# Kernel optimization log

Hardware: AMD Instinct MI355X
Metric: run time of the kernel (lower is better)

## Reference

```python
import jax, jax.numpy as jnp
import numpy as np

STRIDE = 1
PADDING = (1, 1, 1, 1)  # (left, right, top, bottom), as in torch F.pad for last two dims
NEG_INF = -jnp.inf


def maxplus_conv2d(x, kernel, stride=STRIDE):
    """Tropical (max-plus) conv2d, groups=1.
    x: [B, C, H, W] (already padded), kernel: [O, C, kh, kw].
    out[b,o,h,w] = max_{c,ki,kj} x[b,c,h*s+ki,w*s+kj] + kernel[o,c,ki,kj]
    """
    B, C, H, W = x.shape
    O, Cg, kh, kw = kernel.shape
    Ho = (H - kh) // stride + 1
    Wo = (W - kw) // stride + 1
    out = jnp.full((B, O, Ho, Wo), NEG_INF, dtype=x.dtype)
    # Loop over the small, fixed kernel taps (kh*kw = 9); reductions over the
    # channel axis stay fully vectorized and fuse into a single add+reduce-max.
    for ki in range(kh):
        for kj in range(kw):
            xs = x[:, :, ki:ki + Ho * stride:stride, kj:kj + Wo * stride:stride]  # [B,C,Ho,Wo]
            cand = jnp.max(xs[:, None, :, :, :] + kernel[None, :, :, ki, kj][:, :, :, None, None], axis=2)
            out = jnp.maximum(out, cand)
    return out


def setup_inputs() -> dict:
    key = jax.random.key(0)
    kx, kk = jax.random.split(key)
    x = jax.random.normal(kx, (8, 64, 64, 64), dtype=jnp.float32)
    kernel = jax.random.normal(kk, (64, 64, 3, 3), dtype=jnp.float32) * 0.1
    return {"x": x, "kernel": kernel}


def reference(x, kernel):
    left, right, top, bottom = PADDING
    # MaxPlus semifield: pad with the additive identity of max, i.e. -inf
    xp = jnp.pad(x, ((0, 0), (0, 0), (top, bottom), (left, right)), mode="constant", constant_values=NEG_INF)
    return maxplus_conv2d(xp, kernel, STRIDE)
```

## Files before the change

kernel.cpp:

```cpp
#include <hip/hip_runtime.h>

#define NEG_INF (-__builtin_huge_valf())

#define CCH   4
#define HB    4
#define ROWS  (HB + 2)
#define XSTR  64
#define ESTR  40
#define SLOTS 6

__global__ __launch_bounds__(64, 4)
void maxplus_conv2d_kernel(const float* __restrict__ x,
                           const float* __restrict__ kern,
                           float* __restrict__ out) {
    __shared__ float xs[CCH * ROWS * XSTR];
    __shared__ float es[CCH * ROWS * ESTR];

    const int tid = threadIdx.x;
    const int wg  = tid & 15;
    const int hr  = tid >> 4;
    const int w0  = wg << 2;

    const int h_base = blockIdx.x * HB;
    const int b      = blockIdx.y;
    const int o_base = blockIdx.z << 1;

    const float* xb = x + (size_t)b * 64 * 64 * 64;
    const float* gsrc[SLOTS];
    float*       xdst[SLOTS];
    float*       edst[SLOTS];
    bool         vmask[SLOTS];
#pragma unroll
    for (int k = 0; k < SLOTS; ++k) {
        int rowid = k * 4 + hr;
        int cl    = rowid / ROWS;
        int r     = rowid - cl * ROWS;
        int gh    = h_base + r - 1;
        bool valid = (unsigned)gh < 64u;
        int  ghc   = valid ? gh : 0;
        gsrc[k]  = xb + ((size_t)cl * 64 + ghc) * 64 + wg * 4;
        xdst[k]  = &xs[rowid * XSTR + wg * 4];
        edst[k]  = &es[rowid * ESTR + wg];
        vmask[k] = valid;
    }

    if (tid < CCH * ROWS) {
        es[tid * ESTR + 0]  = NEG_INF;
        es[tid * ESTR + 34] = NEG_INF;
    }

    float acc[2][4];
#pragma unroll
    for (int oo = 0; oo < 2; ++oo)
#pragma unroll
        for (int wi = 0; wi < 4; ++wi)
            acc[oo][wi] = NEG_INF;

    float4 R[SLOTS];
#pragma unroll
    for (int k = 0; k < SLOTS; ++k) R[k] = *(const float4*)gsrc[k];

#pragma unroll 1
    for (int cc = 0; cc < 64; cc += CCH) {
        __syncthreads();

#pragma unroll
        for (int k = 0; k < SLOTS; ++k) {
            float4 v = R[k];
            if (!vmask[k]) v = make_float4(NEG_INF, NEG_INF, NEG_INF, NEG_INF);
            *(float4*)xdst[k] = v;
            edst[k][1]  = v.w;
            edst[k][18] = v.x;
        }

        __syncthreads();

        if (cc + CCH < 64) {
#pragma unroll
            for (int k = 0; k < SLOTS; ++k) {
                gsrc[k] += CCH * 64 * 64;
                R[k] = *(const float4*)gsrc[k];
            }
        }

        float kv[CCH][2][9];
#pragma unroll
        for (int cl = 0; cl < CCH; ++cl)
#pragma unroll
            for (int oo = 0; oo < 2; ++oo) {
                const float* kp = kern + ((size_t)(o_base + oo) * 64 + (cc + cl)) * 9;
#pragma unroll
                for (int t = 0; t < 9; ++t) kv[cl][oo][t] = kp[t];
            }

#pragma unroll
        for (int cl = 0; cl < CCH; ++cl) {
            float xv[3][6];
#pragma unroll
            for (int r = 0; r < 3; ++r) {
                const int rowid = cl * ROWS + hr + r;
                float4 m = *(const float4*)(&xs[rowid * XSTR + w0]);
                const float* ep = &es[rowid * ESTR + wg];
                xv[r][0] = ep[0];
                xv[r][5] = ep[19];
                xv[r][1] = m.x; xv[r][2] = m.y; xv[r][3] = m.z; xv[r][4] = m.w;
            }

#pragma unroll
            for (int oo = 0; oo < 2; ++oo) {
                const float* k9 = kv[cl][oo];
#pragma unroll
                for (int wi = 0; wi < 4; ++wi) {
                    float m = acc[oo][wi];
                    float t0 = xv[0][wi + 0] + k9[0];
                    float t1 = xv[0][wi + 1] + k9[1];
                    m = fmaxf(m, fmaxf(t0, t1));
                    t0 = xv[0][wi + 2] + k9[2];
                    t1 = xv[1][wi + 0] + k9[3];
                    m = fmaxf(m, fmaxf(t0, t1));
                    t0 = xv[1][wi + 1] + k9[4];
                    t1 = xv[1][wi + 2] + k9[5];
                    m = fmaxf(m, fmaxf(t0, t1));
                    t0 = xv[2][wi + 0] + k9[6];
                    t1 = xv[2][wi + 1] + k9[7];
                    m = fmaxf(m, fmaxf(t0, t1));
                    m = fmaxf(m, xv[2][wi + 2] + k9[8]);
                    acc[oo][wi] = m;
                }
            }
        }
    }

    const int h = h_base + hr;
#pragma unroll
    for (int oo = 0; oo < 2; ++oo) {
        float4 v = make_float4(acc[oo][0], acc[oo][1], acc[oo][2], acc[oo][3]);
        *(float4*)(out + ((((size_t)b * 64 + (o_base + oo)) * 64 + h) * 64 + w0)) = v;
    }
}

extern "C" void kernel_launch(void* const* d_in, const int* in_sizes, int n_in,
                              void* d_out, int out_size, void* d_ws, size_t ws_size,
                              hipStream_t stream) {
    const float* x    = (const float*)d_in[0];
    const float* kern = (const float*)d_in[1];
    float* out = (float*)d_out;

    dim3 grid(16, 8, 32);
    dim3 block(64);
    maxplus_conv2d_kernel<<<grid, block, 0, stream>>>(x, kern, out);
}
```

Baseline: 110.2 us.

## Share input tile across four waves and fetch halo columns via DPP

Each block now holds four waves, and each wave computes two output channels from a single shared input tile, so input traffic per output channel drops by a factor of four. The channel chunk per stage is doubled to 8. The separate shared-memory edge array is removed and left/right neighbour columns are read across lanes with DPP row shifts that fill -inf at the row boundaries. Padding rows are now written once as -inf for edge blocks instead of being masked on every store. The cost is a larger block, twice the shared memory per block, a split inner loop to limit registers, and fewer blocks in the grid.

After: 123.0 us. 1.12x slower.

```diff
diff --git a/kernel.cpp b/kernel.cpp
--- a/kernel.cpp
+++ b/kernel.cpp
@@ -1,52 +1,60 @@
 #include <hip/hip_runtime.h>
 
 #define NEG_INF (-__builtin_huge_valf())
+#define NEG_INF_BITS 0xFF800000
 
-#define CCH   4
-#define HB    4
-#define ROWS  (HB + 2)
-#define XSTR  64
-#define ESTR  40
-#define SLOTS 6
+#define CCH    8
+#define HB     4
+#define ROWS   (HB + 2)
+#define NROW   (CCH * ROWS)
+#define XSTR   64
+#define SLOTS  3
+#define OW     4
 
-__global__ __launch_bounds__(64, 4)
+template <int CTRL>
+__device__ __forceinline__ float dpp_neighbor(float v) {
+    return __int_as_float(__builtin_amdgcn_update_dpp(
+        (int)NEG_INF_BITS, __float_as_int(v), CTRL, 0xF, 0xF, false));
+}
+
+__global__ __launch_bounds__(256, 4)
 void maxplus_conv2d_kernel(const float* __restrict__ x,
                            const float* __restrict__ kern,
                            float* __restrict__ out) {
-    __shared__ float xs[CCH * ROWS * XSTR];
-    __shared__ float es[CCH * ROWS * ESTR];
+    __shared__ float xs[NROW * XSTR];
 
-    const int tid = threadIdx.x;
-    const int wg  = tid & 15;
-    const int hr  = tid >> 4;
-    const int w0  = wg << 2;
+    const int tid  = threadIdx.x;
+    const int lane = tid & 63;
+    const int wave = __builtin_amdgcn_readfirstlane(tid >> 6);
+    const int wg   = lane & 15;
+    const int hr   = lane >> 4;
+    const int w0   = wg << 2;
 
     const int h_base = blockIdx.x * HB;
     const int b      = blockIdx.y;
-    const int o_base = blockIdx.z << 1;
+    const int o0     = blockIdx.z * (OW * 2) + wave * 2;
 
-    const float* xb = x + (size_t)b * 64 * 64 * 64;
+    if (h_base == 0 || h_base == 60) {
+        for (int k = tid; k < NROW * XSTR; k += 256)
+            xs[k] = NEG_INF;
+    }
+
+    const float* xb = x + (size_t)b * (64 * 64 * 64);
     const float* gsrc[SLOTS];
     float*       xdst[SLOTS];
-    float*       edst[SLOTS];
-    bool         vmask[SLOTS];
+    bool         sval[SLOTS];
 #pragma unroll
-    for (int k = 0; k < SLOTS; ++k) {
-        int rowid = k * 4 + hr;
+    for (int s = 0; s < SLOTS; ++s) {
+        int idx   = s * 256 + tid;
+        int rowid = idx >> 4;
+        int wgp   = idx & 15;
         int cl    = rowid / ROWS;
         int r     = rowid - cl * ROWS;
         int gh    = h_base + r - 1;
-        bool valid = (unsigned)gh < 64u;
-        int  ghc   = valid ? gh : 0;
-        gsrc[k]  = xb + ((size_t)cl * 64 + ghc) * 64 + wg * 4;
-        xdst[k]  = &xs[rowid * XSTR + wg * 4];
-        edst[k]  = &es[rowid * ESTR + wg];
-        vmask[k] = valid;
-    }
-
-    if (tid < CCH * ROWS) {
-        es[tid * ESTR + 0]  = NEG_INF;
-        es[tid * ESTR + 34] = NEG_INF;
+        bool v    = (unsigned)gh < 64u;
+        gsrc[s] = xb + ((size_t)cl * 64 + (v ? gh : 0)) * 64 + wgp * 4;
+        xdst[s] = &xs[rowid * XSTR + wgp * 4];
+        sval[s] = v;
     }
 
     float acc[2][4];
@@ -58,74 +66,71 @@
 
     float4 R[SLOTS];
 #pragma unroll
-    for (int k = 0; k < SLOTS; ++k) R[k] = *(const float4*)gsrc[k];
+    for (int s = 0; s < SLOTS; ++s) R[s] = *(const float4*)gsrc[s];
+
+    const float* kpw = kern + (size_t)o0 * (64 * 9);
 
 #pragma unroll 1
     for (int cc = 0; cc < 64; cc += CCH) {
         __syncthreads();
-
 #pragma unroll
-        for (int k = 0; k < SLOTS; ++k) {
-            float4 v = R[k];
-            if (!vmask[k]) v = make_float4(NEG_INF, NEG_INF, NEG_INF, NEG_INF);
-            *(float4*)xdst[k] = v;
-            edst[k][1]  = v.w;
-            edst[k][18] = v.x;
-        }
-
+        for (int s = 0; s < SLOTS; ++s)
+            if (sval[s]) *(float4*)xdst[s] = R[s];
         __syncthreads();
 
         if (cc + CCH < 64) {
 #pragma unroll
-            for (int k = 0; k < SLOTS; ++k) {
-                gsrc[k] += CCH * 64 * 64;
-                R[k] = *(const float4*)gsrc[k];
+            for (int s = 0; s < SLOTS; ++s) {
+                gsrc[s] += CCH * 64 * 64;
+                R[s] = *(const float4*)gsrc[s];
             }
         }
 
-        float kv[CCH][2][9];
+#pragma unroll 1
+        for (int half = 0; half < 2; ++half) {
+            float kv[4][2][9];
 #pragma unroll
-        for (int cl = 0; cl < CCH; ++cl)
+            for (int cl = 0; cl < 4; ++cl)
 #pragma unroll
-            for (int oo = 0; oo < 2; ++oo) {
-                const float* kp = kern + ((size_t)(o_base + oo) * 64 + (cc + cl)) * 9;
+                for (int oo = 0; oo < 2; ++oo) {
+                    const float* kp = kpw + ((size_t)oo * 64 + (cc + half * 4 + cl)) * 9;
 #pragma unroll
-                for (int t = 0; t < 9; ++t) kv[cl][oo][t] = kp[t];
-            }
+                    for (int t = 0; t < 9; ++t) kv[cl][oo][t] = kp[t];
+                }
 
 #pragma unroll
-        for (int cl = 0; cl < CCH; ++cl) {
-            float xv[3][6];
+            for (int cl = 0; cl < 4; ++cl) {
+                const int rbase = (half * 4 + cl) * ROWS + hr;
+                float xv[3][6];
 #pragma unroll
-            for (int r = 0; r < 3; ++r) {
-                const int rowid = cl * ROWS + hr + r;
-                float4 m = *(const float4*)(&xs[rowid * XSTR + w0]);
-                const float* ep = &es[rowid * ESTR + wg];
-                xv[r][0] = ep[0];
-                xv[r][5] = ep[19];
-                xv[r][1] = m.x; xv[r][2] = m.y; xv[r][3] = m.z; xv[r][4] = m.w;
-            }
+                for (int r = 0; r < 3; ++r) {
+                    float4 m = *(const float4*)(&xs[(rbase + r) * XSTR + w0]);
+                    xv[r][0] = dpp_neighbor<0x111>(m.w);
+                    xv[r][1] = m.x; xv[r][2] = m.y; xv[r][3] = m.z; xv[r][4] = m.w;
+                    xv[r][5] = dpp_neighbor<0x101>(m.x);
+                }
 
 #pragma unroll
-            for (int oo = 0; oo < 2; ++oo) {
-                const float* k9 = kv[cl][oo];
+                for (int oo = 0; oo < 2; ++oo) {
+                    const float* k9 = kv[cl][oo];
 #pragma unroll
-                for (int wi = 0; wi < 4; ++wi) {
-                    float m = acc[oo][wi];
-                    float t0 = xv[0][wi + 0] + k9[0];
-                    float t1 = xv[0][wi + 1] + k9[1];
-                    m = fmaxf(m, fmaxf(t0, t1));
-                    t0 = xv[0][wi + 2] + k9[2];
-                    t1 = xv[1][wi + 0] + k9[3];
-                    m = fmaxf(m, fmaxf(t0, t1));
-                    t0 = xv[1][wi + 1] + k9[4];
-                    t1 = xv[1][wi + 2] + k9[5];
-                    m = fmaxf(m, fmaxf(t0, t1));
-                    t0 = xv[2][wi + 0] + k9[6];
-                    t1 = xv[2][wi + 1] + k9[7];
-                    m = fmaxf(m, fmaxf(t0, t1));
-                    m = fmaxf(m, xv[2][wi + 2] + k9[8]);
-                    acc[oo][wi] = m;
+                    for (int wi = 0; wi < 4; ++wi) {
+                        float m = acc[oo][wi];
+                        float t0 = xv[0][wi + 0] + k9[0];
+                        float t1 = xv[0][wi + 1] + k9[1];
+                        m = fmaxf(m, fmaxf(t0, t1));
+                        t0 = xv[0][wi + 2] + k9[2];
+                        t1 = xv[1][wi + 0] + k9[3];
+                        m = fmaxf(m, fmaxf(t0, t1));
+                        t0 = xv[1][wi + 1] + k9[4];
+                        t1 = xv[1][wi + 2] + k9[5];
+                        m = fmaxf(m, fmaxf(t0, t1));
+                        t0 = xv[2][wi + 0] + k9[6];
+                        t1 = xv[2][wi + 1] + k9[7];
+                        m = fmaxf(m, fmaxf(t0, t1));
+                        m = fmaxf(m, xv[2][wi + 2] + k9[8]);
+                        acc[oo][wi] = m;
+                    }
                 }
             }
         }
@@ -135,7 +140,7 @@
 #pragma unroll
     for (int oo = 0; oo < 2; ++oo) {
         float4 v = make_float4(acc[oo][0], acc[oo][1], acc[oo][2], acc[oo][3]);
-        *(float4*)(out + ((((size_t)b * 64 + (o_base + oo)) * 64 + h) * 64 + w0)) = v;
+        *(float4*)(out + ((((size_t)b * 64 + (o0 + oo)) * 64 + h) * 64 + w0)) = v;
     }
 }
 
@@ -146,7 +151,7 @@
     const float* kern = (const float*)d_in[1];
     float* out = (float*)d_out;
 
-    dim3 grid(16, 8, 32);
-    dim3 block(64);
+    dim3 grid(16, 8, 8);
+    dim3 block(256);
     maxplus_conv2d_kernel<<<grid, block, 0, stream>>>(x, kern, out);
 }
```

## Double-buffer input tiles via async global-to-LDS loads and DPP halo exchange

Applied to the files above, without the earlier changes.

Input rows now go straight from global memory into a double-buffered LDS tile with global_load_lds. The register-staged copy and one barrier per channel chunk are gone, and the next chunk's load overlaps the current chunk's compute. The separate edge-halo shared array is replaced by DPP row shifts, which fetch left and right neighbour values across lanes and fill the border with -inf. Top and bottom padding rows are overwritten with -inf in LDS only for blocks on the image edges. The cost is double the LDS use, and correctness depends on the one-wave block and the DPP row layout lining up with the 16-lane column groups.

New measurement: 134.3 us. 21.9% more time.

```diff
diff --git a/kernel.cpp b/kernel.cpp
--- a/kernel.cpp
+++ b/kernel.cpp
@@ -1,20 +1,26 @@
 #include <hip/hip_runtime.h>
 
 #define NEG_INF (-__builtin_huge_valf())
+#define NEG_INF_BITS 0xFF800000
 
 #define CCH   4
 #define HB    4
 #define ROWS  (HB + 2)
-#define XSTR  64
-#define ESTR  40
+#define NROW  (CCH * ROWS)
+#define BUF   (NROW * 64)
 #define SLOTS 6
+
+template <int CTRL>
+__device__ __forceinline__ float dpp_neighbor(float v) {
+    return __int_as_float(__builtin_amdgcn_update_dpp(
+        (int)NEG_INF_BITS, __float_as_int(v), CTRL, 0xF, 0xF, false));
+}
 
 __global__ __launch_bounds__(64, 4)
 void maxplus_conv2d_kernel(const float* __restrict__ x,
                            const float* __restrict__ kern,
                            float* __restrict__ out) {
-    __shared__ float xs[CCH * ROWS * XSTR];
-    __shared__ float es[CCH * ROWS * ESTR];
+    __shared__ float xs[2 * BUF];
 
     const int tid = threadIdx.x;
     const int wg  = tid & 15;
@@ -25,10 +31,11 @@
     const int b      = blockIdx.y;
     const int o_base = blockIdx.z << 1;
 
-    const float* xb = x + (size_t)b * 64 * 64 * 64;
+    const bool hedge = (h_base == 0) || (h_base == 60);
+
+    const float* xb = x + (size_t)b * (64 * 64 * 64);
     const float* gsrc[SLOTS];
-    float*       xdst[SLOTS];
-    float*       edst[SLOTS];
+    int          foff[SLOTS];
     bool         vmask[SLOTS];
 #pragma unroll
     for (int k = 0; k < SLOTS; ++k) {
@@ -36,17 +43,10 @@
         int cl    = rowid / ROWS;
         int r     = rowid - cl * ROWS;
         int gh    = h_base + r - 1;
-        bool valid = (unsigned)gh < 64u;
-        int  ghc   = valid ? gh : 0;
-        gsrc[k]  = xb + ((size_t)cl * 64 + ghc) * 64 + wg * 4;
-        xdst[k]  = &xs[rowid * XSTR + wg * 4];
-        edst[k]  = &es[rowid * ESTR + wg];
-        vmask[k] = valid;
-    }
-
-    if (tid < CCH * ROWS) {
-        es[tid * ESTR + 0]  = NEG_INF;
-        es[tid * ESTR + 34] = NEG_INF;
+        bool v    = (unsigned)gh < 64u;
+        gsrc[k]  = xb + ((size_t)cl * 64 + (v ? gh : 0)) * 64 + wg * 4;
+        foff[k]  = k * 256 + tid * 4;
+        vmask[k] = v;
     }
 
     float acc[2][4];
@@ -56,31 +56,36 @@
         for (int wi = 0; wi < 4; ++wi)
             acc[oo][wi] = NEG_INF;
 
-    float4 R[SLOTS];
 #pragma unroll
-    for (int k = 0; k < SLOTS; ++k) R[k] = *(const float4*)gsrc[k];
+    for (int k = 0; k < SLOTS; ++k)
+        __builtin_amdgcn_global_load_lds(
+            (const __attribute__((address_space(1))) void*)gsrc[k],
+            (__attribute__((address_space(3))) void*)&xs[k * 256], 16, 0, 0);
+    asm volatile("s_waitcnt vmcnt(0)" ::: "memory");
+    __syncthreads();
 
+    int cur = 0;
 #pragma unroll 1
     for (int cc = 0; cc < 64; cc += CCH) {
-        __syncthreads();
-
-#pragma unroll
-        for (int k = 0; k < SLOTS; ++k) {
-            float4 v = R[k];
-            if (!vmask[k]) v = make_float4(NEG_INF, NEG_INF, NEG_INF, NEG_INF);
-            *(float4*)xdst[k] = v;
-            edst[k][1]  = v.w;
-            edst[k][18] = v.x;
-        }
-
-        __syncthreads();
-
         if (cc + CCH < 64) {
 #pragma unroll
             for (int k = 0; k < SLOTS; ++k) {
                 gsrc[k] += CCH * 64 * 64;
-                R[k] = *(const float4*)gsrc[k];
+                __builtin_amdgcn_global_load_lds(
+                    (const __attribute__((address_space(1))) void*)gsrc[k],
+                    (__attribute__((address_space(3))) void*)
+                        &xs[(cur ^ 1) * BUF + k * 256], 16, 0, 0);
             }
+        }
+
+        float* bp = &xs[cur * BUF];
+
+        if (hedge) {
+#pragma unroll
+            for (int k = 0; k < SLOTS; ++k)
+                if (!vmask[k])
+                    *(float4*)(bp + foff[k]) =
+                        make_float4(NEG_INF, NEG_INF, NEG_INF, NEG_INF);
         }
 
         float kv[CCH][2][9];
@@ -99,11 +104,10 @@
 #pragma unroll
             for (int r = 0; r < 3; ++r) {
                 const int rowid = cl * ROWS + hr + r;
-                float4 m = *(const float4*)(&xs[rowid * XSTR + w0]);
-                const float* ep = &es[rowid * ESTR + wg];
-                xv[r][0] = ep[0];
-                xv[r][5] = ep[19];
+                float4 m = *(const float4*)(bp + rowid * 64 + w0);
+                xv[r][0] = dpp_neighbor<0x111>(m.w);
                 xv[r][1] = m.x; xv[r][2] = m.y; xv[r][3] = m.z; xv[r][4] = m.w;
+                xv[r][5] = dpp_neighbor<0x101>(m.x);
             }
 
 #pragma unroll
@@ -129,6 +133,10 @@
                 }
             }
         }
+
+        asm volatile("s_waitcnt vmcnt(0)" ::: "memory");
+        __syncthreads();
+        cur ^= 1;
     }
 
     const int h = h_base + hr;
```

## Compute four output channels per block and fetch row neighbors via DPP

Applied to the files above, without the earlier changes.

Each block now computes four output channels instead of two, so every staged input tile is reused across twice as many channels, and the grid is halved. The separate edge shared-memory array, which held neighbor values across thread boundaries, is removed. Left and right halo values are now exchanged between adjacent lanes with DPP row shifts, which fill NEG_INF at row boundaries as the padding. In exchange, each thread holds more accumulators and the occupancy hint drops, which means fewer waves are available to hide latency.

New measurement: 121.2 us. +10.1%, slower.

```diff
diff --git a/kernel.cpp b/kernel.cpp
--- a/kernel.cpp
+++ b/kernel.cpp
@@ -1,20 +1,48 @@
 #include <hip/hip_runtime.h>
 
 #define NEG_INF (-__builtin_huge_valf())
+#define NEG_INF_BITS 0xFF800000
 
 #define CCH   4
 #define HB    4
 #define ROWS  (HB + 2)
+#define NROW  (CCH * ROWS)
 #define XSTR  64
-#define ESTR  40
 #define SLOTS 6
 
-__global__ __launch_bounds__(64, 4)
+template <int CTRL>
+__device__ __forceinline__ float dpp_neighbor(float v) {
+    return __int_as_float(__builtin_amdgcn_update_dpp(
+        (int)NEG_INF_BITS, __float_as_int(v), CTRL, 0xF, 0xF, false));
+}
+
+__device__ __forceinline__ void maxplus9(const float xv[3][6], const float* k9,
+                                         float a[4]) {
+#pragma unroll
+    for (int wi = 0; wi < 4; ++wi) {
+        float m = a[wi];
+        float t0 = xv[0][wi + 0] + k9[0];
+        float t1 = xv[0][wi + 1] + k9[1];
+        m = fmaxf(m, fmaxf(t0, t1));
+        t0 = xv[0][wi + 2] + k9[2];
+        t1 = xv[1][wi + 0] + k9[3];
+        m = fmaxf(m, fmaxf(t0, t1));
+        t0 = xv[1][wi + 1] + k9[4];
+        t1 = xv[1][wi + 2] + k9[5];
+        m = fmaxf(m, fmaxf(t0, t1));
+        t0 = xv[2][wi + 0] + k9[6];
+        t1 = xv[2][wi + 1] + k9[7];
+        m = fmaxf(m, fmaxf(t0, t1));
+        m = fmaxf(m, xv[2][wi + 2] + k9[8]);
+        a[wi] = m;
+    }
+}
+
+__global__ __launch_bounds__(64, 2)
 void maxplus_conv2d_kernel(const float* __restrict__ x,
                            const float* __restrict__ kern,
                            float* __restrict__ out) {
-    __shared__ float xs[CCH * ROWS * XSTR];
-    __shared__ float es[CCH * ROWS * ESTR];
+    __shared__ float xs[NROW * XSTR];
 
     const int tid = threadIdx.x;
     const int wg  = tid & 15;
@@ -23,12 +51,11 @@
 
     const int h_base = blockIdx.x * HB;
     const int b      = blockIdx.y;
-    const int o_base = blockIdx.z << 1;
+    const int o_base = blockIdx.z << 2;
 
-    const float* xb = x + (size_t)b * 64 * 64 * 64;
+    const float* xb = x + (size_t)b * (64 * 64 * 64);
     const float* gsrc[SLOTS];
     float*       xdst[SLOTS];
-    float*       edst[SLOTS];
     bool         vmask[SLOTS];
 #pragma unroll
     for (int k = 0; k < SLOTS; ++k) {
@@ -36,22 +63,15 @@
         int cl    = rowid / ROWS;
         int r     = rowid - cl * ROWS;
         int gh    = h_base + r - 1;
-        bool valid = (unsigned)gh < 64u;
-        int  ghc   = valid ? gh : 0;
-        gsrc[k]  = xb + ((size_t)cl * 64 + ghc) * 64 + wg * 4;
+        bool v    = (unsigned)gh < 64u;
+        gsrc[k]  = xb + ((size_t)cl * 64 + (v ? gh : 0)) * 64 + wg * 4;
         xdst[k]  = &xs[rowid * XSTR + wg * 4];
-        edst[k]  = &es[rowid * ESTR + wg];
-        vmask[k] = valid;
+        vmask[k] = v;
     }
 
-    if (tid < CCH * ROWS) {
-        es[tid * ESTR + 0]  = NEG_INF;
-        es[tid * ESTR + 34] = NEG_INF;
-    }
-
-    float acc[2][4];
+    float acc[4][4];
 #pragma unroll
-    for (int oo = 0; oo < 2; ++oo)
+    for (int oo = 0; oo < 4; ++oo)
 #pragma unroll
         for (int wi = 0; wi < 4; ++wi)
             acc[oo][wi] = NEG_INF;
@@ -69,8 +89,6 @@
             float4 v = R[k];
             if (!vmask[k]) v = make_float4(NEG_INF, NEG_INF, NEG_INF, NEG_INF);
             *(float4*)xdst[k] = v;
-            edst[k][1]  = v.w;
-            edst[k][18] = v.x;
         }
 
         __syncthreads();
@@ -83,57 +101,39 @@
             }
         }
 
-        float kv[CCH][2][9];
 #pragma unroll
-        for (int cl = 0; cl < CCH; ++cl)
+        for (int op = 0; op < 2; ++op) {
+            float kv[CCH][2][9];
 #pragma unroll
-            for (int oo = 0; oo < 2; ++oo) {
-                const float* kp = kern + ((size_t)(o_base + oo) * 64 + (cc + cl)) * 9;
+            for (int cl = 0; cl < CCH; ++cl)
 #pragma unroll
-                for (int t = 0; t < 9; ++t) kv[cl][oo][t] = kp[t];
-            }
+                for (int oo = 0; oo < 2; ++oo) {
+                    const float* kp =
+                        kern + ((size_t)(o_base + op * 2 + oo) * 64 + (cc + cl)) * 9;
+#pragma unroll
+                    for (int t = 0; t < 9; ++t) kv[cl][oo][t] = kp[t];
+                }
 
 #pragma unroll
-        for (int cl = 0; cl < CCH; ++cl) {
-            float xv[3][6];
+            for (int cl = 0; cl < CCH; ++cl) {
+                float xv[3][6];
 #pragma unroll
-            for (int r = 0; r < 3; ++r) {
-                const int rowid = cl * ROWS + hr + r;
-                float4 m = *(const float4*)(&xs[rowid * XSTR + w0]);
-                const float* ep = &es[rowid * ESTR + wg];
-                xv[r][0] = ep[0];
-                xv[r][5] = ep[19];
-                xv[r][1] = m.x; xv[r][2] = m.y; xv[r][3] = m.z; xv[r][4] = m.w;
-            }
-
-#pragma unroll
-            for (int oo = 0; oo < 2; ++oo) {
-                const float* k9 = kv[cl][oo];
-#pragma unroll
-                for (int wi = 0; wi < 4; ++wi) {
-                    float m = acc[oo][wi];
-                    float t0 = xv[0][wi + 0] + k9[0];
-                    float t1 = xv[0][wi + 1] + k9[1];
-                    m = fmaxf(m, fmaxf(t0, t1));
-                    t0 = xv[0][wi + 2] + k9[2];
-                    t1 = xv[1][wi + 0] + k9[3];
-                    m = fmaxf(m, fmaxf(t0, t1));
-                    t0 = xv[1][wi + 1] + k9[4];
-                    t1 = xv[1][wi + 2] + k9[5];
-                    m = fmaxf(m, fmaxf(t0, t1));
-                    t0 = xv[2][wi + 0] + k9[6];
-                    t1 = xv[2][wi + 1] + k9[7];
-                    m = fmaxf(m, fmaxf(t0, t1));
-                    m = fmaxf(m, xv[2][wi + 2] + k9[8]);
-                    acc[oo][wi] = m;
+                for (int r = 0; r < 3; ++r) {
+                    const int rowid = cl * ROWS + hr + r;
+                    float4 m = *(const float4*)(&xs[rowid * XSTR + w0]);
+                    xv[r][0] = dpp_neighbor<0x111>(m.w);
+                    xv[r][1] = m.x; xv[r][2] = m.y; xv[r][3] = m.z; xv[r][4] = m.w;
+                    xv[r][5] = dpp_neighbor<0x101>(m.x);
                 }
+                maxplus9(xv, kv[cl][0], acc[op * 2 + 0]);
+                maxplus9(xv, kv[cl][1], acc[op * 2 + 1]);
             }
         }
     }
 
     const int h = h_base + hr;
 #pragma unroll
-    for (int oo = 0; oo < 2; ++oo) {
+    for (int oo = 0; oo < 4; ++oo) {
         float4 v = make_float4(acc[oo][0], acc[oo][1], acc[oo][2], acc[oo][3]);
         *(float4*)(out + ((((size_t)b * 64 + (o_base + oo)) * 64 + h) * 64 + w0)) = v;
     }
@@ -146,7 +146,7 @@
     const float* kern = (const float*)d_in[1];
     float* out = (float*)d_out;
 
-    dim3 grid(16, 8, 32);
+    dim3 grid(16, 8, 16);
     dim3 block(64);
     maxplus_conv2d_kernel<<<grid, block, 0, stream>>>(x, kern, out);
 }
```
